# Optimization experiments

Hardware: AMD Instinct MI355X
Metric: run time of the kernel (lower is better)

Reference implementation:

```python
import jax, jax.numpy as jnp
import numpy as np

N = 100000   # active voxels/points
C = 64       # channels
K = 27       # kernel_size^3 offsets
EPS = 1e-5   # BatchNorm eps (torch default)


def setup_inputs() -> dict:
    key = jax.random.key(0)
    ks = jax.random.split(key, 6)
    x = jax.random.normal(ks[0], (N, C), dtype=jnp.float32)
    norm_points = jax.random.uniform(ks[1], (N, 3), dtype=jnp.float32)
    in_idx = jax.random.randint(ks[2], (K, N), 0, N)
    out_idx = jax.random.randint(ks[3], (K, N), 0, N)
    scale = 1.0 / np.sqrt(K * C).astype(np.float32)
    W1 = jax.random.normal(ks[4], (K, C, C), dtype=jnp.float32) * scale
    W2 = jax.random.normal(ks[5], (K, C, C), dtype=jnp.float32) * scale
    gamma1 = jnp.ones((C,), jnp.float32)
    beta1 = jnp.zeros((C,), jnp.float32)
    gamma2 = jnp.ones((C,), jnp.float32)
    beta2 = jnp.zeros((C,), jnp.float32)
    return dict(x=x, norm_points=norm_points, W1=W1, gamma1=gamma1, beta1=beta1,
                W2=W2, gamma2=gamma2, beta2=beta2, in_idx=in_idx, out_idx=out_idx)


def _sparse_conv(x, W, in_idx, out_idx):
    # gather-GEMM-scatter sparse conv:
    # x: [N, Cin], W: [K, Cin, Cout], in_idx/out_idx: [K, E]
    msgs = jnp.einsum('kec,kcd->ked', x[in_idx], W)          # [K, E, Cout]
    return jax.ops.segment_sum(msgs.reshape(-1, msgs.shape[-1]),
                               out_idx.reshape(-1), num_segments=x.shape[0])


def _batch_norm(x, gamma, beta):
    # BN over all points (training-mode batch stats, biased variance)
    mu = x.mean(axis=0)
    var = x.var(axis=0)
    return (x - mu) * jax.lax.rsqrt(var + EPS) * gamma + beta


def reference(x, norm_points, W1, gamma1, beta1, W2, gamma2, beta2, in_idx, out_idx):
    # layer1 -> BN -> ReLU
    out = jax.nn.relu(_batch_norm(_sparse_conv(x, W1, in_idx, out_idx), gamma1, beta1))
    # layer2 -> BN -> +residual -> ReLU
    out = _batch_norm(_sparse_conv(out, W2, in_idx, out_idx), gamma2, beta2)
    return jax.nn.relu(out + x)
```

## Files before the change

### kernel.cpp

```cpp
#include <hip/hip_runtime.h>

#define NPTS 100000
#define CC   64
#define KK   27
#define TOT  (KK * NPTS)
#define EPSBN 1e-5f
#define MT   128
#define NB   ((NPTS + MT - 1) / MT)
#define CAP  200

#define CHUNK  12500
#define NCH    (TOT / CHUNK)

#define XBLK   (NPTS * CC / 1024)
#define WBLK   (2 * KK * CC * CC / 256)

#define FPSCALE 262144.0f
#define FPINV   3.814697265625e-06f
#define FPMAGIC 12582912.0f
#define FPBITS  0x4B400000

typedef float          f32x4  __attribute__((ext_vector_type(4)));
typedef short          bf16x8 __attribute__((ext_vector_type(8)));
typedef unsigned int   u32x4  __attribute__((ext_vector_type(4)));
typedef unsigned short u16x4  __attribute__((ext_vector_type(4)));
typedef int            i32x4  __attribute__((ext_vector_type(4)));

__device__ __forceinline__ unsigned short f2bf(float f) {
    unsigned int u = __float_as_uint(f);
    u = (u + 0x7fffu + ((u >> 16) & 1u)) >> 16;
    return (unsigned short)u;
}

__device__ __forceinline__ int f2fix(float v) {
    return __float_as_int(fmaf(v, FPSCALE, FPMAGIC)) - FPBITS;
}

__global__ void k_prep(const float* __restrict__ x,
                       const float* __restrict__ W1, const float* __restrict__ W2,
                       unsigned short* __restrict__ xb,
                       unsigned short* __restrict__ Wt1, unsigned short* __restrict__ Wt2) {
    int b = blockIdx.x;
    if (b < XBLK) {
        int id = b * 256 + threadIdx.x;
        f32x4 v = ((const f32x4*)x)[id];
        u16x4 o;
#pragma unroll
        for (int j = 0; j < 4; ++j) o[j] = f2bf(v[j]);
        ((u16x4*)xb)[id] = o;
    } else {
        int id = (b - XBLK) * 256 + threadIdx.x;
        int which = id / (KK * CC * CC);
        int r = id % (KK * CC * CC);
        int k = r / (CC * CC);
        int rem = r % (CC * CC);
        int cin = rem / CC, cout = rem % CC;
        const float* W = which ? W2 : W1;
        unsigned short* Wt = which ? Wt2 : Wt1;
        Wt[k * CC * CC + cout * CC + cin] = f2bf(W[r]);
    }
}

__global__ __launch_bounds__(256) void k_part(
    const int* __restrict__ out_idx, const int* __restrict__ in_idx,
    int* __restrict__ cnt, unsigned* __restrict__ entries) {
    __shared__ int lc[NB];
    const int t = threadIdx.x;
    for (int i = t; i < NB; i += 256) lc[i] = 0;
    __syncthreads();
    const int j0 = blockIdx.x * CHUNK;
    const int k  = j0 / NPTS;
    const i32x4* dsrc = (const i32x4*)(out_idx + j0);
    const i32x4* ssrc = (const i32x4*)(in_idx + j0);
    for (int ii = t; ii < CHUNK / 4; ii += 256) {
        i32x4 d = dsrc[ii];
#pragma unroll
        for (int q = 0; q < 4; ++q) atomicAdd(&lc[d[q] >> 7], 1);
    }
    __syncthreads();
    for (int i = t; i < NB; i += 256)
        lc[i] = atomicAdd(&cnt[k * NB + i], lc[i]);
    __syncthreads();
    for (int ii = t; ii < CHUNK / 4; ii += 256) {
        i32x4 d4 = dsrc[ii];
        i32x4 s4 = ssrc[ii];
#pragma unroll
        for (int q = 0; q < 4; ++q) {
            int d = d4[q];
            int b = d >> 7;
            int pos = atomicAdd(&lc[b], 1);
            if (pos < CAP)
                entries[(k * NB + b) * CAP + pos] =
                    ((unsigned)(d & 127) << 17) | (unsigned)s4[q];
        }
    }
}

__global__ __launch_bounds__(512, 4) void k_conv(
    const unsigned short* __restrict__ xb,
    const unsigned short* __restrict__ Wt,
    const int* __restrict__ cnt,
    const unsigned* __restrict__ entries,
    float* __restrict__ y,
    float* __restrict__ sums)
{
    __shared__ int ylds[MT * 64];

    const int tid  = threadIdx.x;
    const int lane = tid & 63;
    const int wave = tid >> 6;
    const int quad = lane >> 4;
    const int l16  = lane & 15;
    const int blk  = blockIdx.x;
    const int i0   = blk << 7;

    for (int i = tid; i < MT * 64; i += 512) ylds[i] = 0;
    __syncthreads();

    const unsigned short* xq = xb + quad * 8;

    for (int k = wave; k < KK; k += 8) {
        const int bkt   = k * NB + blk;
        const int start = bkt * CAP;
        int E = cnt[bkt];
        E = E > CAP ? CAP : E;
        if (E == 0) continue;
        const int emax = E - 1;

        bf16x8 bfr[4][2];
        const unsigned short* wk = Wt + k * (CC * CC) + l16 * CC + quad * 8;
#pragma unroll
        for (int nt = 0; nt < 4; ++nt) {
            bfr[nt][0] = *(const bf16x8*)(wk + nt * 16 * CC);
            bfr[nt][1] = *(const bf16x8*)(wk + nt * 16 * CC + 32);
        }

        const int ntile = (E + 31) >> 5;

        unsigned eA0 = entries[start + min(l16, emax)];
        unsigned eB0 = entries[start + min(16 + l16, emax)];
        bf16x8 fc[2][2], fn[2][2];
        {
            const unsigned short* p0 = xq + (eA0 & 0x1FFFFu) * CC;
            const unsigned short* p1 = xq + (eB0 & 0x1FFFFu) * CC;
            fc[0][0] = *(const bf16x8*)p0;
            fc[0][1] = *(const bf16x8*)(p0 + 32);
            fc[1][0] = *(const bf16x8*)p1;
            fc[1][1] = *(const bf16x8*)(p1 + 32);
        }
        unsigned eA1 = entries[start + min(32 + l16, emax)];
        unsigned eB1 = entries[start + min(48 + l16, emax)];
        {
            const unsigned short* p0 = xq + (eA1 & 0x1FFFFu) * CC;
            const unsigned short* p1 = xq + (eB1 & 0x1FFFFu) * CC;
            fn[0][0] = *(const bf16x8*)p0;
            fn[0][1] = *(const bf16x8*)(p0 + 32);
            fn[1][0] = *(const bf16x8*)p1;
            fn[1][1] = *(const bf16x8*)(p1 + 32);
        }
        unsigned eA2 = entries[start + min(64 + l16, emax)];
        unsigned eB2 = entries[start + min(80 + l16, emax)];

        for (int t = 0; t < ntile; ++t) {
            const int tb = t * 32;
            unsigned dp[2][4];
#pragma unroll
            for (int rr = 0; rr < 4; ++rr) {
                dp[0][rr] = (unsigned)__shfl((int)eA0, quad * 4 + rr, 16);
                dp[1][rr] = (unsigned)__shfl((int)eB0, quad * 4 + rr, 16);
            }
            bf16x8 fp[2][2];
            {
                const unsigned short* p0 = xq + (eA2 & 0x1FFFFu) * CC;
                const unsigned short* p1 = xq + (eB2 & 0x1FFFFu) * CC;
                fp[0][0] = *(const bf16x8*)p0;
                fp[0][1] = *(const bf16x8*)(p0 + 32);
                fp[1][0] = *(const bf16x8*)p1;
                fp[1][1] = *(const bf16x8*)(p1 + 32);
            }
            unsigned eA3 = entries[start + min(tb + 96 + l16, emax)];
            unsigned eB3 = entries[start + min(tb + 112 + l16, emax)];

            f32x4 acc[2][4];
#pragma unroll
            for (int mt = 0; mt < 2; ++mt)
#pragma unroll
                for (int nt = 0; nt < 4; ++nt) acc[mt][nt] = (f32x4){0.f, 0.f, 0.f, 0.f};
            __builtin_amdgcn_s_setprio(1);
#pragma unroll
            for (int mt = 0; mt < 2; ++mt)
#pragma unroll
                for (int nt = 0; nt < 4; ++nt) {
                    acc[mt][nt] = __builtin_amdgcn_mfma_f32_16x16x32_bf16(
                        fc[mt][0], bfr[nt][0], acc[mt][nt], 0, 0, 0);
                    acc[mt][nt] = __builtin_amdgcn_mfma_f32_16x16x32_bf16(
                        fc[mt][1], bfr[nt][1], acc[mt][nt], 0, 0, 0);
                }
            __builtin_amdgcn_s_setprio(0);

#pragma unroll
            for (int mt = 0; mt < 2; ++mt)
#pragma unroll
                for (int rr = 0; rr < 4; ++rr) {
                    int slot = tb + mt * 16 + quad * 4 + rr;
                    if (slot < E) {
                        int row = (int)(dp[mt][rr] >> 17);
                        int xv = (row & 1) << 4;
                        unsigned* yp = (unsigned*)&ylds[row * 64 + l16];
                        atomicAdd(yp + (0 ^ xv),  (unsigned)f2fix(acc[mt][0][rr]));
                        atomicAdd(yp + (16 ^ xv), (unsigned)f2fix(acc[mt][1][rr]));
                        atomicAdd(yp + (32 ^ xv), (unsigned)f2fix(acc[mt][2][rr]));
                        atomicAdd(yp + (48 ^ xv), (unsigned)f2fix(acc[mt][3][rr]));
                    }
                }
            fc[0][0] = fn[0][0]; fc[0][1] = fn[0][1];
            fc[1][0] = fn[1][0]; fc[1][1] = fn[1][1];
            fn[0][0] = fp[0][0]; fn[0][1] = fp[0][1];
            fn[1][0] = fp[1][0]; fn[1][1] = fp[1][1];
            eA0 = eA1; eB0 = eB1;
            eA1 = eA2; eB1 = eB2;
            eA2 = eA3; eB2 = eB3;
        }
    }
    __syncthreads();

    const int col = tid & 63;
    const int rg  = tid >> 6;
    float s = 0.f, q = 0.f;
#pragma unroll
    for (int i = 0; i < 16; ++i) {
        int row = rg * 16 + i;
        float v = (float)ylds[row * 64 + (col ^ ((row & 1) << 4))] * FPINV;
        int gr = i0 + row;
        if (gr < NPTS) y[(long)gr * CC + col] = v;
        s += v; q += v * v;
    }
    __syncthreads();
    float* ps = (float*)ylds;
    ps[rg * 128 + col] = s;
    ps[rg * 128 + 64 + col] = q;
    __syncthreads();
    if (tid < 128) {
        int which = tid >> 6, c = tid & 63;
        float a = 0.f;
#pragma unroll
        for (int wv = 0; wv < 8; ++wv) a += ps[wv * 128 + which * 64 + c];
        atomicAdd(&sums[which * 64 + c], a);
    }
}

__global__ void k_apply(const float* __restrict__ y, const float* __restrict__ sums,
                        const float* __restrict__ gamma, const float* __restrict__ beta,
                        unsigned short* __restrict__ ab) {
    __shared__ float sb[128];
    int t = threadIdx.x;
    if (t < 64) {
        float mu  = sums[t] * (1.0f / NPTS);
        float var = sums[t + 64] * (1.0f / NPTS) - mu * mu;
        float s = gamma[t] * rsqrtf(var + EPSBN);
        sb[t] = s;
        sb[t + 64] = beta[t] - mu * s;
    }
    __syncthreads();
    int id = blockIdx.x * 256 + t;
    f32x4 v = ((const f32x4*)y)[id];
    int c0 = (id * 4) & 63;
    u16x4 o;
#pragma unroll
    for (int j = 0; j < 4; ++j) {
        float r = fmaxf(v[j] * sb[c0 + j] + sb[64 + c0 + j], 0.f);
        o[j] = f2bf(r);
    }
    ((u16x4*)ab)[id] = o;
}

__global__ void k_final(const float* __restrict__ y, const float* __restrict__ x,
                        const float* __restrict__ sums,
                        const float* __restrict__ gamma, const float* __restrict__ beta,
                        float* __restrict__ out) {
    __shared__ float sb[128];
    int t = threadIdx.x;
    if (t < 64) {
        float mu  = sums[t] * (1.0f / NPTS);
        float var = sums[t + 64] * (1.0f / NPTS) - mu * mu;
        float s = gamma[t] * rsqrtf(var + EPSBN);
        sb[t] = s;
        sb[t + 64] = beta[t] - mu * s;
    }
    __syncthreads();
    int id = blockIdx.x * 256 + t;
    f32x4 v  = ((const f32x4*)y)[id];
    f32x4 xv = ((const f32x4*)x)[id];
    int c0 = (id * 4) & 63;
    f32x4 o;
#pragma unroll
    for (int j = 0; j < 4; ++j)
        o[j] = fmaxf(v[j] * sb[c0 + j] + sb[64 + c0 + j] + xv[j], 0.f);
    ((f32x4*)out)[id] = o;
}

extern "C" void kernel_launch(void* const* d_in, const int* in_sizes, int n_in,
                              void* d_out, int out_size, void* d_ws, size_t ws_size,
                              hipStream_t stream) {
    const float* x      = (const float*)d_in[0];
    const float* W1     = (const float*)d_in[2];
    const float* gamma1 = (const float*)d_in[3];
    const float* beta1  = (const float*)d_in[4];
    const float* W2     = (const float*)d_in[5];
    const float* gamma2 = (const float*)d_in[6];
    const float* beta2  = (const float*)d_in[7];
    const int* in_idx   = (const int*)d_in[8];
    const int* out_idx  = (const int*)d_in[9];
    float* out = (float*)d_out;

    char* w = (char*)d_ws;
    size_t off = 0;
    auto alloc = [&](size_t bytes) -> char* {
        off = (off + 255) & ~(size_t)255;
        char* p = w + off;
        off += bytes;
        return p;
    };
    int*   cnt       = (int*)     alloc((size_t)KK * NB * 4);
    float* sums      = (float*)   alloc(256 * 4);
    unsigned* entries = (unsigned*)alloc((size_t)KK * NB * CAP * 4);
    unsigned short* xbf = (unsigned short*)alloc((size_t)NPTS * CC * 2);
    unsigned short* Wt1 = (unsigned short*)alloc((size_t)KK * CC * CC * 2);
    unsigned short* Wt2 = (unsigned short*)alloc((size_t)KK * CC * CC * 2);
    float* y = (float*)alloc((size_t)NPTS * CC * 4);

    size_t zlen = (size_t)((char*)(sums + 256) - (char*)cnt);
    hipMemsetAsync(cnt, 0, zlen, stream);

    k_prep<<<XBLK + WBLK, 256, 0, stream>>>(x, W1, W2, xbf, Wt1, Wt2);
    k_part<<<NCH, 256, 0, stream>>>(out_idx, in_idx, cnt, entries);

    k_conv<<<NB, 512, 0, stream>>>(xbf, Wt1, cnt, entries, y, sums);
    k_apply<<<NPTS * CC / 1024, 256, 0, stream>>>(y, sums, gamma1, beta1, xbf);
    k_conv<<<NB, 512, 0, stream>>>(xbf, Wt2, cnt, entries, y, sums + 128);
    k_final<<<NPTS * CC / 1024, 256, 0, stream>>>(y, x, sums + 128, gamma2, beta2, out);
}
```

Before: 366.3 us.

## Split conv buckets into source-index phases with block barriers to improve gather locality

Each (offset, output-tile) bucket is split into three sub-buckets by which third of the source-point range the input index falls in. The conv kernel processes the phases in order with a block-wide barrier between them, so concurrently running blocks gather from roughly the same third of the bf16 activation array and share cache. This adds a division per entry in partitioning and more bucket setup and barriers in the conv. Per-phase capacity is also smaller, which raises the risk of silently dropping entries from overflowing buckets.

```diff
diff --git a/kernel.cpp b/kernel.cpp
--- a/kernel.cpp
+++ b/kernel.cpp
@@ -7,7 +7,8 @@
 #define EPSBN 1e-5f
 #define MT   128
 #define NB   ((NPTS + MT - 1) / MT)
-#define CAP  200
+#define PH   3
+#define CAPP 88
 
 #define CHUNK  12500
 #define NCH    (TOT / CHUNK)
@@ -64,22 +65,26 @@
 __global__ __launch_bounds__(256) void k_part(
     const int* __restrict__ out_idx, const int* __restrict__ in_idx,
     int* __restrict__ cnt, unsigned* __restrict__ entries) {
-    __shared__ int lc[NB];
+    __shared__ int lc[NB * PH];
     const int t = threadIdx.x;
-    for (int i = t; i < NB; i += 256) lc[i] = 0;
+    for (int i = t; i < NB * PH; i += 256) lc[i] = 0;
     __syncthreads();
     const int j0 = blockIdx.x * CHUNK;
     const int k  = j0 / NPTS;
     const i32x4* dsrc = (const i32x4*)(out_idx + j0);
     const i32x4* ssrc = (const i32x4*)(in_idx + j0);
     for (int ii = t; ii < CHUNK / 4; ii += 256) {
-        i32x4 d = dsrc[ii];
-#pragma unroll
-        for (int q = 0; q < 4; ++q) atomicAdd(&lc[d[q] >> 7], 1);
-    }
-    __syncthreads();
-    for (int i = t; i < NB; i += 256)
-        lc[i] = atomicAdd(&cnt[k * NB + i], lc[i]);
+        i32x4 d4 = dsrc[ii];
+        i32x4 s4 = ssrc[ii];
+#pragma unroll
+        for (int q = 0; q < 4; ++q) {
+            int ph = (s4[q] * 3) / NPTS;
+            atomicAdd(&lc[(d4[q] >> 7) * PH + ph], 1);
+        }
+    }
+    __syncthreads();
+    for (int i = t; i < NB * PH; i += 256)
+        lc[i] = atomicAdd(&cnt[k * NB * PH + i], lc[i]);
     __syncthreads();
     for (int ii = t; ii < CHUNK / 4; ii += 256) {
         i32x4 d4 = dsrc[ii];
@@ -87,11 +92,12 @@
 #pragma unroll
         for (int q = 0; q < 4; ++q) {
             int d = d4[q];
-            int b = d >> 7;
-            int pos = atomicAdd(&lc[b], 1);
-            if (pos < CAP)
-                entries[(k * NB + b) * CAP + pos] =
-                    ((unsigned)(d & 127) << 17) | (unsigned)s4[q];
+            int s = s4[q];
+            int sb = (d >> 7) * PH + (s * 3) / NPTS;
+            int pos = atomicAdd(&lc[sb], 1);
+            if (pos < CAPP)
+                entries[((size_t)k * NB * PH + sb) * CAPP + pos] =
+                    ((unsigned)(d & 127) << 17) | (unsigned)s;
         }
     }
 }
@@ -119,110 +125,112 @@
 
     const unsigned short* xq = xb + quad * 8;
 
-    for (int k = wave; k < KK; k += 8) {
-        const int bkt   = k * NB + blk;
-        const int start = bkt * CAP;
-        int E = cnt[bkt];
-        E = E > CAP ? CAP : E;
-        if (E == 0) continue;
-        const int emax = E - 1;
-
-        bf16x8 bfr[4][2];
-        const unsigned short* wk = Wt + k * (CC * CC) + l16 * CC + quad * 8;
-#pragma unroll
-        for (int nt = 0; nt < 4; ++nt) {
-            bfr[nt][0] = *(const bf16x8*)(wk + nt * 16 * CC);
-            bfr[nt][1] = *(const bf16x8*)(wk + nt * 16 * CC + 32);
+    for (int ph = 0; ph < PH; ++ph) {
+        for (int k = wave; k < KK; k += 8) {
+            const size_t sb = (size_t)(k * NB + blk) * PH + ph;
+            const size_t start = sb * CAPP;
+            int E = cnt[sb];
+            E = E > CAPP ? CAPP : E;
+            if (E == 0) continue;
+            const int emax = E - 1;
+
+            bf16x8 bfr[4][2];
+            const unsigned short* wk = Wt + k * (CC * CC) + l16 * CC + quad * 8;
+#pragma unroll
+            for (int nt = 0; nt < 4; ++nt) {
+                bfr[nt][0] = *(const bf16x8*)(wk + nt * 16 * CC);
+                bfr[nt][1] = *(const bf16x8*)(wk + nt * 16 * CC + 32);
+            }
+
+            const int ntile = (E + 31) >> 5;
+
+            unsigned eA0 = entries[start + min(l16, emax)];
+            unsigned eB0 = entries[start + min(16 + l16, emax)];
+            bf16x8 fc[2][2], fn[2][2];
+            {
+                const unsigned short* p0 = xq + (eA0 & 0x1FFFFu) * CC;
+                const unsigned short* p1 = xq + (eB0 & 0x1FFFFu) * CC;
+                fc[0][0] = *(const bf16x8*)p0;
+                fc[0][1] = *(const bf16x8*)(p0 + 32);
+                fc[1][0] = *(const bf16x8*)p1;
+                fc[1][1] = *(const bf16x8*)(p1 + 32);
+            }
+            unsigned eA1 = entries[start + min(32 + l16, emax)];
+            unsigned eB1 = entries[start + min(48 + l16, emax)];
+            {
+                const unsigned short* p0 = xq + (eA1 & 0x1FFFFu) * CC;
+                const unsigned short* p1 = xq + (eB1 & 0x1FFFFu) * CC;
+                fn[0][0] = *(const bf16x8*)p0;
+                fn[0][1] = *(const bf16x8*)(p0 + 32);
+                fn[1][0] = *(const bf16x8*)p1;
+                fn[1][1] = *(const bf16x8*)(p1 + 32);
+            }
+            unsigned eA2 = entries[start + min(64 + l16, emax)];
+            unsigned eB2 = entries[start + min(80 + l16, emax)];
+
+            for (int t = 0; t < ntile; ++t) {
+                const int tb = t * 32;
+                unsigned dp[2][4];
+#pragma unroll
+                for (int rr = 0; rr < 4; ++rr) {
+                    dp[0][rr] = (unsigned)__shfl((int)eA0, quad * 4 + rr, 16);
+                    dp[1][rr] = (unsigned)__shfl((int)eB0, quad * 4 + rr, 16);
+                }
+                bf16x8 fp[2][2];
+                {
+                    const unsigned short* p0 = xq + (eA2 & 0x1FFFFu) * CC;
+                    const unsigned short* p1 = xq + (eB2 & 0x1FFFFu) * CC;
+                    fp[0][0] = *(const bf16x8*)p0;
+                    fp[0][1] = *(const bf16x8*)(p0 + 32);
+                    fp[1][0] = *(const bf16x8*)p1;
+                    fp[1][1] = *(const bf16x8*)(p1 + 32);
+                }
+                unsigned eA3 = entries[start + min(tb + 96 + l16, emax)];
+                unsigned eB3 = entries[start + min(tb + 112 + l16, emax)];
+
+                f32x4 acc[2][4];
+#pragma unroll
+                for (int mt = 0; mt < 2; ++mt)
+#pragma unroll
+                    for (int nt = 0; nt < 4; ++nt) acc[mt][nt] = (f32x4){0.f, 0.f, 0.f, 0.f};
+                __builtin_amdgcn_s_setprio(1);
+#pragma unroll
+                for (int mt = 0; mt < 2; ++mt)
+#pragma unroll
+                    for (int nt = 0; nt < 4; ++nt) {
+                        acc[mt][nt] = __builtin_amdgcn_mfma_f32_16x16x32_bf16(
+                            fc[mt][0], bfr[nt][0], acc[mt][nt], 0, 0, 0);
+                        acc[mt][nt] = __builtin_amdgcn_mfma_f32_16x16x32_bf16(
+                            fc[mt][1], bfr[nt][1], acc[mt][nt], 0, 0, 0);
+                    }
+                __builtin_amdgcn_s_setprio(0);
+
+#pragma unroll
+                for (int mt = 0; mt < 2; ++mt)
+#pragma unroll
+                    for (int rr = 0; rr < 4; ++rr) {
+                        int slot = tb + mt * 16 + quad * 4 + rr;
+                        if (slot < E) {
+                            int row = (int)(dp[mt][rr] >> 17);
+                            int xv = (row & 1) << 4;
+                            unsigned* yp = (unsigned*)&ylds[row * 64 + l16];
+                            atomicAdd(yp + (0 ^ xv),  (unsigned)f2fix(acc[mt][0][rr]));
+                            atomicAdd(yp + (16 ^ xv), (unsigned)f2fix(acc[mt][1][rr]));
+                            atomicAdd(yp + (32 ^ xv), (unsigned)f2fix(acc[mt][2][rr]));
+                            atomicAdd(yp + (48 ^ xv), (unsigned)f2fix(acc[mt][3][rr]));
+                        }
+                    }
+                fc[0][0] = fn[0][0]; fc[0][1] = fn[0][1];
+                fc[1][0] = fn[1][0]; fc[1][1] = fn[1][1];
+                fn[0][0] = fp[0][0]; fn[0][1] = fp[0][1];
+                fn[1][0] = fp[1][0]; fn[1][1] = fp[1][1];
+                eA0 = eA1; eB0 = eB1;
+                eA1 = eA2; eB1 = eB2;
+                eA2 = eA3; eB2 = eB3;
+            }
         }
-
-        const int ntile = (E + 31) >> 5;
-
-        unsigned eA0 = entries[start + min(l16, emax)];
-        unsigned eB0 = entries[start + min(16 + l16, emax)];
-        bf16x8 fc[2][2], fn[2][2];
-        {
-            const unsigned short* p0 = xq + (eA0 & 0x1FFFFu) * CC;
-            const unsigned short* p1 = xq + (eB0 & 0x1FFFFu) * CC;
-            fc[0][0] = *(const bf16x8*)p0;
-            fc[0][1] = *(const bf16x8*)(p0 + 32);
-            fc[1][0] = *(const bf16x8*)p1;
-            fc[1][1] = *(const bf16x8*)(p1 + 32);
-        }
-        unsigned eA1 = entries[start + min(32 + l16, emax)];
-        unsigned eB1 = entries[start + min(48 + l16, emax)];
-        {
-            const unsigned short* p0 = xq + (eA1 & 0x1FFFFu) * CC;
-            const unsigned short* p1 = xq + (eB1 & 0x1FFFFu) * CC;
-            fn[0][0] = *(const bf16x8*)p0;
-            fn[0][1] = *(const bf16x8*)(p0 + 32);
-            fn[1][0] = *(const bf16x8*)p1;
-            fn[1][1] = *(const bf16x8*)(p1 + 32);
-        }
-        unsigned eA2 = entries[start + min(64 + l16, emax)];
-        unsigned eB2 = entries[start + min(80 + l16, emax)];
-
-        for (int t = 0; t < ntile; ++t) {
-            const int tb = t * 32;
-            unsigned dp[2][4];
-#pragma unroll
-            for (int rr = 0; rr < 4; ++rr) {
-                dp[0][rr] = (unsigned)__shfl((int)eA0, quad * 4 + rr, 16);
-                dp[1][rr] = (unsigned)__shfl((int)eB0, quad * 4 + rr, 16);
-            }
-            bf16x8 fp[2][2];
-            {
-                const unsigned short* p0 = xq + (eA2 & 0x1FFFFu) * CC;
-                const unsigned short* p1 = xq + (eB2 & 0x1FFFFu) * CC;
-                fp[0][0] = *(const bf16x8*)p0;
-                fp[0][1] = *(const bf16x8*)(p0 + 32);
-                fp[1][0] = *(const bf16x8*)p1;
-                fp[1][1] = *(const bf16x8*)(p1 + 32);
-            }
-            unsigned eA3 = entries[start + min(tb + 96 + l16, emax)];
-            unsigned eB3 = entries[start + min(tb + 112 + l16, emax)];
-
-            f32x4 acc[2][4];
-#pragma unroll
-            for (int mt = 0; mt < 2; ++mt)
-#pragma unroll
-                for (int nt = 0; nt < 4; ++nt) acc[mt][nt] = (f32x4){0.f, 0.f, 0.f, 0.f};
-            __builtin_amdgcn_s_setprio(1);
-#pragma unroll
-            for (int mt = 0; mt < 2; ++mt)
-#pragma unroll
-                for (int nt = 0; nt < 4; ++nt) {
-                    acc[mt][nt] = __builtin_amdgcn_mfma_f32_16x16x32_bf16(
-                        fc[mt][0], bfr[nt][0], acc[mt][nt], 0, 0, 0);
-                    acc[mt][nt] = __builtin_amdgcn_mfma_f32_16x16x32_bf16(
-                        fc[mt][1], bfr[nt][1], acc[mt][nt], 0, 0, 0);
-                }
-            __builtin_amdgcn_s_setprio(0);
-
-#pragma unroll
-            for (int mt = 0; mt < 2; ++mt)
-#pragma unroll
-                for (int rr = 0; rr < 4; ++rr) {
-                    int slot = tb + mt * 16 + quad * 4 + rr;
-                    if (slot < E) {
-                        int row = (int)(dp[mt][rr] >> 17);
-                        int xv = (row & 1) << 4;
-                        unsigned* yp = (unsigned*)&ylds[row * 64 + l16];
-                        atomicAdd(yp + (0 ^ xv),  (unsigned)f2fix(acc[mt][0][rr]));
-                        atomicAdd(yp + (16 ^ xv), (unsigned)f2fix(acc[mt][1][rr]));
-                        atomicAdd(yp + (32 ^ xv), (unsigned)f2fix(acc[mt][2][rr]));
-                        atomicAdd(yp + (48 ^ xv), (unsigned)f2fix(acc[mt][3][rr]));
-                    }
-                }
-            fc[0][0] = fn[0][0]; fc[0][1] = fn[0][1];
-            fc[1][0] = fn[1][0]; fc[1][1] = fn[1][1];
-            fn[0][0] = fp[0][0]; fn[0][1] = fp[0][1];
-            fn[1][0] = fp[1][0]; fn[1][1] = fp[1][1];
-            eA0 = eA1; eB0 = eB1;
-            eA1 = eA2; eB1 = eB2;
-            eA2 = eA3; eB2 = eB3;
-        }
-    }
-    __syncthreads();
+        __syncthreads();
+    }
 
     const int col = tid & 63;
     const int rg  = tid >> 6;
@@ -321,9 +329,9 @@
         off += bytes;
         return p;
     };
-    int*   cnt       = (int*)     alloc((size_t)KK * NB * 4);
+    int*   cnt       = (int*)     alloc((size_t)KK * NB * PH * 4);
     float* sums      = (float*)   alloc(256 * 4);
-    unsigned* entries = (unsigned*)alloc((size_t)KK * NB * CAP * 4);
+    unsigned* entries = (unsigned*)alloc((size_t)KK * NB * PH * CAPP * 4);
     unsigned short* xbf = (unsigned short*)alloc((size_t)NPTS * CC * 2);
     unsigned short* Wt1 = (unsigned short*)alloc((size_t)KK * CC * CC * 2);
     unsigned short* Wt2 = (unsigned short*)alloc((size_t)KK * CC * CC * 2);
```

New measurement: 507.8 us. 38.6% more time.

## Merge prep and partition kernels; double-buffer gather pipeline in conv loop

Applied to the files above, without the earlier changes.

Fuses the bf16 conversion/weight-transpose kernel with the bucket partition kernel into one launch, which removes a kernel boundary. The conv inner loop becomes a manually unrolled ping-pong across two fragment buffers, with sched_barrier fences so the next tile's gather is issued before the current tile's MFMAs. The MFMA chain now starts from a constant zero accumulator instead of explicitly zeroed registers. This cuts prefetch depth from two tiles ahead to one, which may expose more gather latency, and adds scheduling constraints.

```diff
diff --git a/kernel.cpp b/kernel.cpp
--- a/kernel.cpp
+++ b/kernel.cpp
@@ -36,20 +36,27 @@
     return __float_as_int(fmaf(v, FPSCALE, FPMAGIC)) - FPBITS;
 }
 
-__global__ void k_prep(const float* __restrict__ x,
-                       const float* __restrict__ W1, const float* __restrict__ W2,
-                       unsigned short* __restrict__ xb,
-                       unsigned short* __restrict__ Wt1, unsigned short* __restrict__ Wt2) {
+__global__ __launch_bounds__(256) void k_prep_part(
+    const float* __restrict__ x,
+    const float* __restrict__ W1, const float* __restrict__ W2,
+    const int* __restrict__ out_idx, const int* __restrict__ in_idx,
+    unsigned short* __restrict__ xb,
+    unsigned short* __restrict__ Wt1, unsigned short* __restrict__ Wt2,
+    int* __restrict__ cnt, unsigned* __restrict__ entries) {
+    __shared__ int lc[NB];
+    const int t = threadIdx.x;
     int b = blockIdx.x;
     if (b < XBLK) {
-        int id = b * 256 + threadIdx.x;
+        int id = b * 256 + t;
         f32x4 v = ((const f32x4*)x)[id];
         u16x4 o;
 #pragma unroll
         for (int j = 0; j < 4; ++j) o[j] = f2bf(v[j]);
         ((u16x4*)xb)[id] = o;
-    } else {
-        int id = (b - XBLK) * 256 + threadIdx.x;
+        return;
+    }
+    if (b < XBLK + WBLK) {
+        int id = (b - XBLK) * 256 + t;
         int which = id / (KK * CC * CC);
         int r = id % (KK * CC * CC);
         int k = r / (CC * CC);
@@ -58,17 +65,12 @@
         const float* W = which ? W2 : W1;
         unsigned short* Wt = which ? Wt2 : Wt1;
         Wt[k * CC * CC + cout * CC + cin] = f2bf(W[r]);
-    }
-}
-
-__global__ __launch_bounds__(256) void k_part(
-    const int* __restrict__ out_idx, const int* __restrict__ in_idx,
-    int* __restrict__ cnt, unsigned* __restrict__ entries) {
-    __shared__ int lc[NB];
-    const int t = threadIdx.x;
+        return;
+    }
+    b -= XBLK + WBLK;
     for (int i = t; i < NB; i += 256) lc[i] = 0;
     __syncthreads();
-    const int j0 = blockIdx.x * CHUNK;
+    const int j0 = b * CHUNK;
     const int k  = j0 / NPTS;
     const i32x4* dsrc = (const i32x4*)(out_idx + j0);
     const i32x4* ssrc = (const i32x4*)(in_idx + j0);
@@ -87,10 +89,10 @@
 #pragma unroll
         for (int q = 0; q < 4; ++q) {
             int d = d4[q];
-            int b = d >> 7;
-            int pos = atomicAdd(&lc[b], 1);
+            int bb = d >> 7;
+            int pos = atomicAdd(&lc[bb], 1);
             if (pos < CAP)
-                entries[(k * NB + b) * CAP + pos] =
+                entries[(size_t)(k * NB + bb) * CAP + pos] =
                     ((unsigned)(d & 127) << 17) | (unsigned)s4[q];
         }
     }
@@ -118,10 +120,58 @@
     __syncthreads();
 
     const unsigned short* xq = xb + quad * 8;
+    const f32x4 z4 = (f32x4){0.f, 0.f, 0.f, 0.f};
+
+#define GATHER(F, ea, eb)                                        \
+    {                                                            \
+        const unsigned short* p0 = xq + ((ea) & 0x1FFFFu) * CC;  \
+        const unsigned short* p1 = xq + ((eb) & 0x1FFFFu) * CC;  \
+        F[0][0] = *(const bf16x8*)p0;                            \
+        F[0][1] = *(const bf16x8*)(p0 + 32);                     \
+        F[1][0] = *(const bf16x8*)p1;                            \
+        F[1][1] = *(const bf16x8*)(p1 + 32);                     \
+    }
+
+#define TILE_COMPUTE(F, ca, cb, tb)                                             \
+    {                                                                           \
+        unsigned dp[2][4];                                                      \
+        _Pragma("unroll")                                                       \
+        for (int rr = 0; rr < 4; ++rr) {                                        \
+            dp[0][rr] = (unsigned)__shfl((int)(ca), quad * 4 + rr, 16);         \
+            dp[1][rr] = (unsigned)__shfl((int)(cb), quad * 4 + rr, 16);         \
+        }                                                                       \
+        f32x4 acc[2][4];                                                        \
+        __builtin_amdgcn_s_setprio(1);                                          \
+        _Pragma("unroll")                                                       \
+        for (int mt = 0; mt < 2; ++mt)                                          \
+            _Pragma("unroll")                                                   \
+            for (int nt = 0; nt < 4; ++nt) {                                    \
+                acc[mt][nt] = __builtin_amdgcn_mfma_f32_16x16x32_bf16(          \
+                    F[mt][0], bfr[nt][0], z4, 0, 0, 0);                         \
+                acc[mt][nt] = __builtin_amdgcn_mfma_f32_16x16x32_bf16(          \
+                    F[mt][1], bfr[nt][1], acc[mt][nt], 0, 0, 0);                \
+            }                                                                   \
+        __builtin_amdgcn_s_setprio(0);                                          \
+        _Pragma("unroll")                                                       \
+        for (int mt = 0; mt < 2; ++mt)                                          \
+            _Pragma("unroll")                                                   \
+            for (int rr = 0; rr < 4; ++rr) {                                    \
+                int slot = (tb) + mt * 16 + quad * 4 + rr;                      \
+                if (slot < E) {                                                 \
+                    int row = (int)(dp[mt][rr] >> 17);                          \
+                    int xv = (row & 1) << 4;                                    \
+                    unsigned* yp = (unsigned*)&ylds[row * 64 + l16];            \
+                    atomicAdd(yp + (0 ^ xv),  (unsigned)f2fix(acc[mt][0][rr])); \
+                    atomicAdd(yp + (16 ^ xv), (unsigned)f2fix(acc[mt][1][rr])); \
+                    atomicAdd(yp + (32 ^ xv), (unsigned)f2fix(acc[mt][2][rr])); \
+                    atomicAdd(yp + (48 ^ xv), (unsigned)f2fix(acc[mt][3][rr])); \
+                }                                                               \
+            }                                                                   \
+    }
 
     for (int k = wave; k < KK; k += 8) {
         const int bkt   = k * NB + blk;
-        const int start = bkt * CAP;
+        const size_t start = (size_t)bkt * CAP;
         int E = cnt[bkt];
         E = E > CAP ? CAP : E;
         if (E == 0) continue;
@@ -137,91 +187,34 @@
 
         const int ntile = (E + 31) >> 5;
 
-        unsigned eA0 = entries[start + min(l16, emax)];
-        unsigned eB0 = entries[start + min(16 + l16, emax)];
-        bf16x8 fc[2][2], fn[2][2];
-        {
-            const unsigned short* p0 = xq + (eA0 & 0x1FFFFu) * CC;
-            const unsigned short* p1 = xq + (eB0 & 0x1FFFFu) * CC;
-            fc[0][0] = *(const bf16x8*)p0;
-            fc[0][1] = *(const bf16x8*)(p0 + 32);
-            fc[1][0] = *(const bf16x8*)p1;
-            fc[1][1] = *(const bf16x8*)(p1 + 32);
+        unsigned a0 = entries[start + min(l16, emax)];
+        unsigned b0 = entries[start + min(16 + l16, emax)];
+        unsigned a1 = entries[start + min(32 + l16, emax)];
+        unsigned b1 = entries[start + min(48 + l16, emax)];
+        bf16x8 fA[2][2], fB[2][2];
+        GATHER(fA, a0, b0);
+
+        int t = 0;
+        while (true) {
+            unsigned a2 = entries[start + min(t * 32 + 64 + l16, emax)];
+            unsigned b2 = entries[start + min(t * 32 + 80 + l16, emax)];
+            GATHER(fB, a1, b1);
+            __builtin_amdgcn_sched_barrier(0);
+            TILE_COMPUTE(fA, a0, b0, t * 32);
+            if (++t >= ntile) break;
+            a0 = a1; b0 = b1; a1 = a2; b1 = b2;
+
+            unsigned a3 = entries[start + min(t * 32 + 64 + l16, emax)];
+            unsigned b3 = entries[start + min(t * 32 + 80 + l16, emax)];
+            GATHER(fA, a1, b1);
+            __builtin_amdgcn_sched_barrier(0);
+            TILE_COMPUTE(fB, a0, b0, t * 32);
+            if (++t >= ntile) break;
+            a0 = a1; b0 = b1; a1 = a3; b1 = b3;
         }
-        unsigned eA1 = entries[start + min(32 + l16, emax)];
-        unsigned eB1 = entries[start + min(48 + l16, emax)];
-        {
-            const unsigned short* p0 = xq + (eA1 & 0x1FFFFu) * CC;
-            const unsigned short* p1 = xq + (eB1 & 0x1FFFFu) * CC;
-            fn[0][0] = *(const bf16x8*)p0;
-            fn[0][1] = *(const bf16x8*)(p0 + 32);
-            fn[1][0] = *(const bf16x8*)p1;
-            fn[1][1] = *(const bf16x8*)(p1 + 32);
-        }
-        unsigned eA2 = entries[start + min(64 + l16, emax)];
-        unsigned eB2 = entries[start + min(80 + l16, emax)];
-
-        for (int t = 0; t < ntile; ++t) {
-            const int tb = t * 32;
-            unsigned dp[2][4];
-#pragma unroll
-            for (int rr = 0; rr < 4; ++rr) {
-                dp[0][rr] = (unsigned)__shfl((int)eA0, quad * 4 + rr, 16);
-                dp[1][rr] = (unsigned)__shfl((int)eB0, quad * 4 + rr, 16);
-            }
-            bf16x8 fp[2][2];
-            {
-                const unsigned short* p0 = xq + (eA2 & 0x1FFFFu) * CC;
-                const unsigned short* p1 = xq + (eB2 & 0x1FFFFu) * CC;
-                fp[0][0] = *(const bf16x8*)p0;
-                fp[0][1] = *(const bf16x8*)(p0 + 32);
-                fp[1][0] = *(const bf16x8*)p1;
-                fp[1][1] = *(const bf16x8*)(p1 + 32);
-            }
-            unsigned eA3 = entries[start + min(tb + 96 + l16, emax)];
-            unsigned eB3 = entries[start + min(tb + 112 + l16, emax)];
-
-            f32x4 acc[2][4];
-#pragma unroll
-            for (int mt = 0; mt < 2; ++mt)
-#pragma unroll
-                for (int nt = 0; nt < 4; ++nt) acc[mt][nt] = (f32x4){0.f, 0.f, 0.f, 0.f};
-            __builtin_amdgcn_s_setprio(1);
-#pragma unroll
-            for (int mt = 0; mt < 2; ++mt)
-#pragma unroll
-                for (int nt = 0; nt < 4; ++nt) {
-                    acc[mt][nt] = __builtin_amdgcn_mfma_f32_16x16x32_bf16(
-                        fc[mt][0], bfr[nt][0], acc[mt][nt], 0, 0, 0);
-                    acc[mt][nt] = __builtin_amdgcn_mfma_f32_16x16x32_bf16(
-                        fc[mt][1], bfr[nt][1], acc[mt][nt], 0, 0, 0);
-                }
-            __builtin_amdgcn_s_setprio(0);
-
-#pragma unroll
-            for (int mt = 0; mt < 2; ++mt)
-#pragma unroll
-                for (int rr = 0; rr < 4; ++rr) {
-                    int slot = tb + mt * 16 + quad * 4 + rr;
-                    if (slot < E) {
-                        int row = (int)(dp[mt][rr] >> 17);
-                        int xv = (row & 1) << 4;
-                        unsigned* yp = (unsigned*)&ylds[row * 64 + l16];
-                        atomicAdd(yp + (0 ^ xv),  (unsigned)f2fix(acc[mt][0][rr]));
-                        atomicAdd(yp + (16 ^ xv), (unsigned)f2fix(acc[mt][1][rr]));
-                        atomicAdd(yp + (32 ^ xv), (unsigned)f2fix(acc[mt][2][rr]));
-                        atomicAdd(yp + (48 ^ xv), (unsigned)f2fix(acc[mt][3][rr]));
-                    }
-                }
-            fc[0][0] = fn[0][0]; fc[0][1] = fn[0][1];
-            fc[1][0] = fn[1][0]; fc[1][1] = fn[1][1];
-            fn[0][0] = fp[0][0]; fn[0][1] = fp[0][1];
-            fn[1][0] = fp[1][0]; fn[1][1] = fp[1][1];
-            eA0 = eA1; eB0 = eB1;
-            eA1 = eA2; eB1 = eB2;
-            eA2 = eA3; eB2 = eB3;
-        }
-    }
+    }
+#undef GATHER
+#undef TILE_COMPUTE
     __syncthreads();
 
     const int col = tid & 63;
@@ -332,8 +325,8 @@
     size_t zlen = (size_t)((char*)(sums + 256) - (char*)cnt);
     hipMemsetAsync(cnt, 0, zlen, stream);
 
-    k_prep<<<XBLK + WBLK, 256, 0, stream>>>(x, W1, W2, xbf, Wt1, Wt2);
-    k_part<<<NCH, 256, 0, stream>>>(out_idx, in_idx, cnt, entries);
+    k_prep_part<<<XBLK + WBLK + NCH, 256, 0, stream>>>(
+        x, W1, W2, out_idx, in_idx, xbf, Wt1, Wt2, cnt, entries);
 
     k_conv<<<NB, 512, 0, stream>>>(xbf, Wt1, cnt, entries, y, sums);
     k_apply<<<NPTS * CC / 1024, 256, 0, stream>>>(y, sums, gamma1, beta1, xbf);
```

Measured after the change: 439.3 us. +19.9%, slower.

## Fuse both convs and BN passes into one persistent kernel with grid barriers

Applied to the files above, without the earlier changes.

Merges the prep and partition kernels into one launch. The two conv, apply and final kernels become a single kernel that keeps each block's accumulator tile in LDS across stages and uses software grid barriers for the BatchNorm statistics. This drops the fp32 y round trip through global memory and several launches. Blocks shrink from 512 to 256 threads (4 waves, each covering more offsets). The grid barrier assumes all 782 blocks are co-resident (4 per CU on 256 CUs), so it risks deadlock or stalls if occupancy falls short.

```diff
diff --git a/kernel.cpp b/kernel.cpp
--- a/kernel.cpp
+++ b/kernel.cpp
@@ -36,20 +36,27 @@
     return __float_as_int(fmaf(v, FPSCALE, FPMAGIC)) - FPBITS;
 }
 
-__global__ void k_prep(const float* __restrict__ x,
-                       const float* __restrict__ W1, const float* __restrict__ W2,
-                       unsigned short* __restrict__ xb,
-                       unsigned short* __restrict__ Wt1, unsigned short* __restrict__ Wt2) {
+__global__ __launch_bounds__(256) void k_prep_part(
+    const float* __restrict__ x,
+    const float* __restrict__ W1, const float* __restrict__ W2,
+    const int* __restrict__ out_idx, const int* __restrict__ in_idx,
+    unsigned short* __restrict__ xb,
+    unsigned short* __restrict__ Wt1, unsigned short* __restrict__ Wt2,
+    int* __restrict__ cnt, unsigned* __restrict__ entries) {
+    __shared__ int lc[NB];
+    const int t = threadIdx.x;
     int b = blockIdx.x;
     if (b < XBLK) {
-        int id = b * 256 + threadIdx.x;
+        int id = b * 256 + t;
         f32x4 v = ((const f32x4*)x)[id];
         u16x4 o;
 #pragma unroll
         for (int j = 0; j < 4; ++j) o[j] = f2bf(v[j]);
         ((u16x4*)xb)[id] = o;
-    } else {
-        int id = (b - XBLK) * 256 + threadIdx.x;
+        return;
+    }
+    if (b < XBLK + WBLK) {
+        int id = (b - XBLK) * 256 + t;
         int which = id / (KK * CC * CC);
         int r = id % (KK * CC * CC);
         int k = r / (CC * CC);
@@ -58,17 +65,12 @@
         const float* W = which ? W2 : W1;
         unsigned short* Wt = which ? Wt2 : Wt1;
         Wt[k * CC * CC + cout * CC + cin] = f2bf(W[r]);
-    }
-}
-
-__global__ __launch_bounds__(256) void k_part(
-    const int* __restrict__ out_idx, const int* __restrict__ in_idx,
-    int* __restrict__ cnt, unsigned* __restrict__ entries) {
-    __shared__ int lc[NB];
-    const int t = threadIdx.x;
+        return;
+    }
+    b -= XBLK + WBLK;
     for (int i = t; i < NB; i += 256) lc[i] = 0;
     __syncthreads();
-    const int j0 = blockIdx.x * CHUNK;
+    const int j0 = b * CHUNK;
     const int k  = j0 / NPTS;
     const i32x4* dsrc = (const i32x4*)(out_idx + j0);
     const i32x4* ssrc = (const i32x4*)(in_idx + j0);
@@ -87,41 +89,27 @@
 #pragma unroll
         for (int q = 0; q < 4; ++q) {
             int d = d4[q];
-            int b = d >> 7;
-            int pos = atomicAdd(&lc[b], 1);
+            int bb = d >> 7;
+            int pos = atomicAdd(&lc[bb], 1);
             if (pos < CAP)
-                entries[(k * NB + b) * CAP + pos] =
+                entries[(size_t)(k * NB + bb) * CAP + pos] =
                     ((unsigned)(d & 127) << 17) | (unsigned)s4[q];
         }
     }
 }
 
-__global__ __launch_bounds__(512, 4) void k_conv(
-    const unsigned short* __restrict__ xb,
+__device__ __forceinline__ void conv_accum(
+    const unsigned short* __restrict__ xsrc,
     const unsigned short* __restrict__ Wt,
     const int* __restrict__ cnt,
     const unsigned* __restrict__ entries,
-    float* __restrict__ y,
-    float* __restrict__ sums)
+    int* ylds, const int blk,
+    const int wave, const int quad, const int l16)
 {
-    __shared__ int ylds[MT * 64];
-
-    const int tid  = threadIdx.x;
-    const int lane = tid & 63;
-    const int wave = tid >> 6;
-    const int quad = lane >> 4;
-    const int l16  = lane & 15;
-    const int blk  = blockIdx.x;
-    const int i0   = blk << 7;
-
-    for (int i = tid; i < MT * 64; i += 512) ylds[i] = 0;
-    __syncthreads();
-
-    const unsigned short* xq = xb + quad * 8;
-
-    for (int k = wave; k < KK; k += 8) {
-        const int bkt   = k * NB + blk;
-        const int start = bkt * CAP;
+    const unsigned short* xq = xsrc + quad * 8;
+    for (int k = wave; k < KK; k += 4) {
+        const int bkt = k * NB + blk;
+        const size_t start = (size_t)bkt * CAP;
         int E = cnt[bkt];
         E = E > CAP ? CAP : E;
         if (E == 0) continue;
@@ -222,81 +210,133 @@
             eA2 = eA3; eB2 = eB3;
         }
     }
-    __syncthreads();
-
-    const int col = tid & 63;
-    const int rg  = tid >> 6;
-    float s = 0.f, q = 0.f;
-#pragma unroll
-    for (int i = 0; i < 16; ++i) {
-        int row = rg * 16 + i;
-        float v = (float)ylds[row * 64 + (col ^ ((row & 1) << 4))] * FPINV;
-        int gr = i0 + row;
-        if (gr < NPTS) y[(long)gr * CC + col] = v;
-        s += v; q += v * v;
-    }
-    __syncthreads();
-    float* ps = (float*)ylds;
-    ps[rg * 128 + col] = s;
-    ps[rg * 128 + 64 + col] = q;
-    __syncthreads();
-    if (tid < 128) {
-        int which = tid >> 6, c = tid & 63;
-        float a = 0.f;
-#pragma unroll
-        for (int wv = 0; wv < 8; ++wv) a += ps[wv * 128 + which * 64 + c];
-        atomicAdd(&sums[which * 64 + c], a);
-    }
-}
-
-__global__ void k_apply(const float* __restrict__ y, const float* __restrict__ sums,
-                        const float* __restrict__ gamma, const float* __restrict__ beta,
-                        unsigned short* __restrict__ ab) {
-    __shared__ float sb[128];
-    int t = threadIdx.x;
-    if (t < 64) {
-        float mu  = sums[t] * (1.0f / NPTS);
-        float var = sums[t + 64] * (1.0f / NPTS) - mu * mu;
-        float s = gamma[t] * rsqrtf(var + EPSBN);
-        sb[t] = s;
-        sb[t + 64] = beta[t] - mu * s;
-    }
-    __syncthreads();
-    int id = blockIdx.x * 256 + t;
-    f32x4 v = ((const f32x4*)y)[id];
-    int c0 = (id * 4) & 63;
-    u16x4 o;
-#pragma unroll
-    for (int j = 0; j < 4; ++j) {
-        float r = fmaxf(v[j] * sb[c0 + j] + sb[64 + c0 + j], 0.f);
-        o[j] = f2bf(r);
-    }
-    ((u16x4*)ab)[id] = o;
-}
-
-__global__ void k_final(const float* __restrict__ y, const float* __restrict__ x,
-                        const float* __restrict__ sums,
-                        const float* __restrict__ gamma, const float* __restrict__ beta,
-                        float* __restrict__ out) {
-    __shared__ float sb[128];
-    int t = threadIdx.x;
-    if (t < 64) {
-        float mu  = sums[t] * (1.0f / NPTS);
-        float var = sums[t + 64] * (1.0f / NPTS) - mu * mu;
-        float s = gamma[t] * rsqrtf(var + EPSBN);
-        sb[t] = s;
-        sb[t + 64] = beta[t] - mu * s;
-    }
-    __syncthreads();
-    int id = blockIdx.x * 256 + t;
-    f32x4 v  = ((const f32x4*)y)[id];
-    f32x4 xv = ((const f32x4*)x)[id];
-    int c0 = (id * 4) & 63;
-    f32x4 o;
-#pragma unroll
-    for (int j = 0; j < 4; ++j)
-        o[j] = fmaxf(v[j] * sb[c0 + j] + sb[64 + c0 + j] + xv[j], 0.f);
-    ((f32x4*)out)[id] = o;
+}
+
+__device__ __forceinline__ void grid_bar(unsigned* bar, unsigned target) {
+    __syncthreads();
+    if (threadIdx.x == 0) {
+        __threadfence();
+        __hip_atomic_fetch_add(bar, 1u, __ATOMIC_RELEASE, __HIP_MEMORY_SCOPE_AGENT);
+        while (__hip_atomic_load(bar, __ATOMIC_ACQUIRE, __HIP_MEMORY_SCOPE_AGENT) < target)
+            __builtin_amdgcn_s_sleep(8);
+    }
+    __syncthreads();
+}
+
+__global__ __launch_bounds__(256, 4) void k_mega(
+    const unsigned short* __restrict__ xb,
+    const unsigned short* __restrict__ Wt1,
+    const unsigned short* __restrict__ Wt2,
+    const int* __restrict__ cnt,
+    const unsigned* __restrict__ entries,
+    unsigned short* __restrict__ a1,
+    const float* __restrict__ x,
+    const float* __restrict__ gamma1, const float* __restrict__ beta1,
+    const float* __restrict__ gamma2, const float* __restrict__ beta2,
+    float* __restrict__ sums,
+    unsigned* __restrict__ bar,
+    float* __restrict__ out)
+{
+    __shared__ int   ylds[MT * 64];
+    __shared__ float ssum[2][4][64];
+
+    const int tid  = threadIdx.x;
+    const int lane = tid & 63;
+    const int wave = tid >> 6;
+    const int quad = lane >> 4;
+    const int l16  = lane & 15;
+    const int blk  = blockIdx.x;
+    const int i0   = blk << 7;
+    const int col  = tid & 63;
+    const int rg   = tid >> 6;
+
+    for (int i = tid; i < MT * 64; i += 256) ylds[i] = 0;
+    __syncthreads();
+
+    conv_accum(xb, Wt1, cnt, entries, ylds, blk, wave, quad, l16);
+    __syncthreads();
+
+    {
+        float s = 0.f, q = 0.f;
+#pragma unroll
+        for (int i = 0; i < 32; ++i) {
+            int row = rg * 32 + i;
+            float v = (float)ylds[row * 64 + (col ^ ((row & 1) << 4))] * FPINV;
+            s += v; q += v * v;
+        }
+        ssum[0][rg][col] = s;
+        ssum[1][rg][col] = q;
+        __syncthreads();
+        if (tid < 128) {
+            int which = tid >> 6, c = tid & 63;
+            float a = ssum[which][0][c] + ssum[which][1][c] +
+                      ssum[which][2][c] + ssum[which][3][c];
+            atomicAdd(&sums[which * 64 + c], a);
+        }
+    }
+    grid_bar(&bar[0], NB);
+
+    {
+        float su = __hip_atomic_load(&sums[col],      __ATOMIC_RELAXED, __HIP_MEMORY_SCOPE_AGENT);
+        float sq = __hip_atomic_load(&sums[64 + col], __ATOMIC_RELAXED, __HIP_MEMORY_SCOPE_AGENT);
+        float mu  = su * (1.0f / NPTS);
+        float var = sq * (1.0f / NPTS) - mu * mu;
+        float sc = gamma1[col] * rsqrtf(var + EPSBN);
+        float bi = beta1[col] - mu * sc;
+#pragma unroll
+        for (int i = 0; i < 32; ++i) {
+            int row = rg * 32 + i;
+            int idx = row * 64 + (col ^ ((row & 1) << 4));
+            float v = (float)ylds[idx] * FPINV;
+            float r = fmaxf(fmaf(v, sc, bi), 0.f);
+            int gr = i0 + row;
+            if (gr < NPTS) a1[(long)gr * CC + col] = f2bf(r);
+            ylds[idx] = 0;
+        }
+    }
+    grid_bar(&bar[1], NB);
+
+    conv_accum(a1, Wt2, cnt, entries, ylds, blk, wave, quad, l16);
+    __syncthreads();
+
+    {
+        float s = 0.f, q = 0.f;
+#pragma unroll
+        for (int i = 0; i < 32; ++i) {
+            int row = rg * 32 + i;
+            float v = (float)ylds[row * 64 + (col ^ ((row & 1) << 4))] * FPINV;
+            s += v; q += v * v;
+        }
+        ssum[0][rg][col] = s;
+        ssum[1][rg][col] = q;
+        __syncthreads();
+        if (tid < 128) {
+            int which = tid >> 6, c = tid & 63;
+            float a = ssum[which][0][c] + ssum[which][1][c] +
+                      ssum[which][2][c] + ssum[which][3][c];
+            atomicAdd(&sums[128 + which * 64 + c], a);
+        }
+    }
+    grid_bar(&bar[2], NB);
+
+    {
+        float su = __hip_atomic_load(&sums[128 + col], __ATOMIC_RELAXED, __HIP_MEMORY_SCOPE_AGENT);
+        float sq = __hip_atomic_load(&sums[192 + col], __ATOMIC_RELAXED, __HIP_MEMORY_SCOPE_AGENT);
+        float mu  = su * (1.0f / NPTS);
+        float var = sq * (1.0f / NPTS) - mu * mu;
+        float sc = gamma2[col] * rsqrtf(var + EPSBN);
+        float bi = beta2[col] - mu * sc;
+#pragma unroll
+        for (int i = 0; i < 32; ++i) {
+            int row = rg * 32 + i;
+            float v = (float)ylds[row * 64 + (col ^ ((row & 1) << 4))] * FPINV;
+            int gr = i0 + row;
+            if (gr < NPTS) {
+                float xv = x[(long)gr * CC + col];
+                out[(long)gr * CC + col] = fmaxf(fmaf(v, sc, bi) + xv, 0.f);
+            }
+        }
+    }
 }
 
 extern "C" void kernel_launch(void* const* d_in, const int* in_sizes, int n_in,
@@ -321,22 +361,22 @@
         off += bytes;
         return p;
     };
-    int*   cnt       = (int*)     alloc((size_t)KK * NB * 4);
-    float* sums      = (float*)   alloc(256 * 4);
+    int*      cnt  = (int*)     alloc((size_t)KK * NB * 4);
+    unsigned* bar  = (unsigned*)alloc(3 * 4);
+    float*    sums = (float*)   alloc(256 * 4);
     unsigned* entries = (unsigned*)alloc((size_t)KK * NB * CAP * 4);
     unsigned short* xbf = (unsigned short*)alloc((size_t)NPTS * CC * 2);
+    unsigned short* a1  = (unsigned short*)alloc((size_t)NPTS * CC * 2);
     unsigned short* Wt1 = (unsigned short*)alloc((size_t)KK * CC * CC * 2);
     unsigned short* Wt2 = (unsigned short*)alloc((size_t)KK * CC * CC * 2);
-    float* y = (float*)alloc((size_t)NPTS * CC * 4);
 
     size_t zlen = (size_t)((char*)(sums + 256) - (char*)cnt);
     hipMemsetAsync(cnt, 0, zlen, stream);
 
-    k_prep<<<XBLK + WBLK, 256, 0, stream>>>(x, W1, W2, xbf, Wt1, Wt2);
-    k_part<<<NCH, 256, 0, stream>>>(out_idx, in_idx, cnt, entries);
-
-    k_conv<<<NB, 512, 0, stream>>>(xbf, Wt1, cnt, entries, y, sums);
-    k_apply<<<NPTS * CC / 1024, 256, 0, stream>>>(y, sums, gamma1, beta1, xbf);
-    k_conv<<<NB, 512, 0, stream>>>(xbf, Wt2, cnt, entries, y, sums + 128);
-    k_final<<<NPTS * CC / 1024, 256, 0, stream>>>(y, x, sums + 128, gamma2, beta2, out);
-}
+    k_prep_part<<<XBLK + WBLK + NCH, 256, 0, stream>>>(
+        x, W1, W2, out_idx, in_idx, xbf, Wt1, Wt2, cnt, entries);
+
+    k_mega<<<NB, 256, 0, stream>>>(
+        xbf, Wt1, Wt2, cnt, entries, a1, x,
+        gamma1, beta1, gamma2, beta2, sums, bar, out);
+}
```

After: 1.117 ms. 205% more time.
